# Performance work log

Hardware: AMD Instinct MI355X
Metric: run time of the kernel (lower is better)

## Reference

```python
import jax, jax.numpy as jnp
import numpy as np

ORDER = 5
LOOKAHEAD = 0
NDF = 96  # n_df_bins


def setup_inputs() -> dict:
    key = jax.random.key(0)
    k1, k2, k3 = jax.random.split(key, 3)
    spec = jax.random.normal(k1, (16, 1, 2000, 481, 2), dtype=jnp.float32)
    coefs = jax.random.normal(k2, (16, 2000, ORDER, NDF, 2), dtype=jnp.float32)
    alpha = jax.random.uniform(k3, (16, 2000, 1), dtype=jnp.float32)
    return {"spec": spec, "coefs": coefs, "alpha": alpha}


def reference(spec, coefs, alpha):
    # spec: [B, 1, T, F, 2]; coefs: [B, T, ORDER, NDF, 2]; alpha: [B, T, 1]
    B, _, T, F, _ = spec.shape
    x = spec[:, 0, :, :NDF, :]  # [B, T, NDF, 2]
    # pad time axis: (order - lookahead - 1) before, lookahead after
    xp = jnp.pad(x, ((0, 0), (ORDER - LOOKAHEAD - 1, LOOKAHEAD), (0, 0), (0, 0)))
    # overlapping time windows of length ORDER (loop over small fixed tap count)
    w = jnp.stack([xp[:, k:k + T] for k in range(ORDER)], axis=2)  # [B, T, ORDER, NDF, 2]
    # complex multiply-accumulate per tap, then sum over taps
    re = w[..., 0] * coefs[..., 0] - w[..., 1] * coefs[..., 1]
    im = w[..., 1] * coefs[..., 0] + w[..., 0] * coefs[..., 1]
    spec_f = jnp.stack((re, im), axis=-1).sum(axis=2)  # [B, T, NDF, 2]
    # alpha blend on the low df_bins, copy the rest unchanged
    a = alpha.reshape(B, 1, T, 1, 1)
    mixed = spec_f[:, None] * a + spec[..., :NDF, :] * (1.0 - a)
    return spec.at[..., :NDF, :].set(mixed)
```

## Files before the change

kernel.cpp:

```cpp
#include <hip/hip_runtime.h>

#define BB 16
#define TT 2000
#define FF 481
#define NDF_ 96
#define ORDER_ 5


__global__ __launch_bounds__(256) void df_op_kernel(
    const float* __restrict__ spec,
    const float* __restrict__ coefs,
    const float* __restrict__ alpha,
    float* __restrict__ out)
{
    const int bt = blockIdx.x;
    const int b  = bt / TT;
    const int t  = bt - b * TT;
    const int tid = threadIdx.x;

    const long row = (long)bt * (FF * 2);
    const float a = alpha[bt];
    const float oma = 1.0f - a;

    if (tid < NDF_) {
        const int f = tid;
        float acc_re = 0.0f, acc_im = 0.0f;
        const float2* cbase = (const float2*)(coefs + (long)bt * (ORDER_ * NDF_ * 2) + f * 2);
        #pragma unroll
        for (int k = 0; k < ORDER_; ++k) {
            const int tk = t - (ORDER_ - 1) + k;
            float2 x = make_float2(0.0f, 0.0f);
            if (tk >= 0) {
                x = *(const float2*)(spec + ((long)b * TT + tk) * (FF * 2) + f * 2);
            }
            const float2 c = cbase[k * NDF_];
            acc_re += x.x * c.x - x.y * c.y;
            acc_im += x.y * c.x + x.x * c.y;
        }
        const float2 s = *(const float2*)(spec + row + f * 2);
        float2 o;
        o.x = acc_re * a + s.x * oma;
        o.y = acc_im * a + s.y * oma;
        *(float2*)(out + row + f * 2) = o;
    }

    const float2* src = (const float2*)(spec + row + NDF_ * 2);
    float2*       dst = (float2*)(out + row + NDF_ * 2);
    for (int i = tid; i < (FF - NDF_); i += 256) {
        dst[i] = src[i];
    }
}

extern "C" void kernel_launch(void* const* d_in, const int* in_sizes, int n_in,
                              void* d_out, int out_size, void* d_ws, size_t ws_size,
                              hipStream_t stream) {
    const float* spec  = (const float*)d_in[0];
    const float* coefs = (const float*)d_in[1];
    const float* alpha = (const float*)d_in[2];
    float* out = (float*)d_out;

    dim3 grid(BB * TT);
    dim3 block(256);
    df_op_kernel<<<grid, block, 0, stream>>>(spec, coefs, alpha, out);
}
```

Measured before the change: 285.9 us.

## Process four time rows per block with vectorized float4 loads and copies

Each block now handles four consecutive (b,t) rows instead of one. Each active thread computes two complex bins, loading coefs as float4, and the tail copy of the untouched bins uses float4 moves with parity-aware alignment plus a float2 edge element. This cuts block count, uses all 256 threads, and widens memory transactions so the bandwidth-bound kernel has fewer, larger accesses. The alignment handling for odd rows adds index arithmetic and could misalign if the row stride assumptions change.

```diff
diff --git a/kernel.cpp b/kernel.cpp
--- a/kernel.cpp
+++ b/kernel.cpp
@@ -5,6 +5,10 @@
 #define FF 481
 #define NDF_ 96
 #define ORDER_ 5
+#define RS (FF * 2)
+#define TILE 4
+#define NV (NDF_ / 2)
+#define CSLOTS 193
 
 
 __global__ __launch_bounds__(256) void df_op_kernel(
@@ -13,41 +17,76 @@
     const float* __restrict__ alpha,
     float* __restrict__ out)
 {
-    const int bt = blockIdx.x;
-    const int b  = bt / TT;
-    const int t  = bt - b * TT;
     const int tid = threadIdx.x;
+    const int bt0 = blockIdx.x * TILE;
+    const int b   = bt0 / TT;
+    const int t0  = bt0 - b * TT;
 
-    const long row = (long)bt * (FF * 2);
-    const float a = alpha[bt];
-    const float oma = 1.0f - a;
+    if (tid < TILE * NV) {
+        const int r  = tid / NV;
+        const int v  = tid - r * NV;
+        const int t  = t0 + r;
+        const int bt = bt0 + r;
 
-    if (tid < NDF_) {
-        const int f = tid;
-        float acc_re = 0.0f, acc_im = 0.0f;
-        const float2* cbase = (const float2*)(coefs + (long)bt * (ORDER_ * NDF_ * 2) + f * 2);
+        float2 xs[ORDER_][2];
         #pragma unroll
         for (int k = 0; k < ORDER_; ++k) {
             const int tk = t - (ORDER_ - 1) + k;
-            float2 x = make_float2(0.0f, 0.0f);
             if (tk >= 0) {
-                x = *(const float2*)(spec + ((long)b * TT + tk) * (FF * 2) + f * 2);
+                const float* p = spec + (size_t)(b * TT + tk) * RS + v * 4;
+                xs[k][0] = *(const float2*)p;
+                xs[k][1] = *(const float2*)(p + 2);
+            } else {
+                xs[k][0] = make_float2(0.0f, 0.0f);
+                xs[k][1] = make_float2(0.0f, 0.0f);
             }
-            const float2 c = cbase[k * NDF_];
-            acc_re += x.x * c.x - x.y * c.y;
-            acc_im += x.y * c.x + x.x * c.y;
         }
-        const float2 s = *(const float2*)(spec + row + f * 2);
-        float2 o;
-        o.x = acc_re * a + s.x * oma;
-        o.y = acc_im * a + s.y * oma;
-        *(float2*)(out + row + f * 2) = o;
+
+        const float4* cp = (const float4*)(coefs + (size_t)bt * (ORDER_ * NDF_ * 2)) + v;
+        float4 cs[ORDER_];
+        #pragma unroll
+        for (int k = 0; k < ORDER_; ++k) cs[k] = cp[(size_t)k * NV];
+
+        float2 a0 = make_float2(0.0f, 0.0f);
+        float2 a1 = make_float2(0.0f, 0.0f);
+        #pragma unroll
+        for (int k = 0; k < ORDER_; ++k) {
+            a0.x += xs[k][0].x * cs[k].x - xs[k][0].y * cs[k].y;
+            a0.y += xs[k][0].y * cs[k].x + xs[k][0].x * cs[k].y;
+            a1.x += xs[k][1].x * cs[k].z - xs[k][1].y * cs[k].w;
+            a1.y += xs[k][1].y * cs[k].z + xs[k][1].x * cs[k].w;
+        }
+
+        const float a   = alpha[bt];
+        const float oma = 1.0f - a;
+        float2 o0, o1;
+        o0.x = a0.x * a + xs[ORDER_ - 1][0].x * oma;
+        o0.y = a0.y * a + xs[ORDER_ - 1][0].y * oma;
+        o1.x = a1.x * a + xs[ORDER_ - 1][1].x * oma;
+        o1.y = a1.y * a + xs[ORDER_ - 1][1].y * oma;
+
+        float* op = out + (size_t)bt * RS + v * 4;
+        *(float2*)op       = o0;
+        *(float2*)(op + 2) = o1;
     }
 
-    const float2* src = (const float2*)(spec + row + NDF_ * 2);
-    float2*       dst = (float2*)(out + row + NDF_ * 2);
-    for (int i = tid; i < (FF - NDF_); i += 256) {
-        dst[i] = src[i];
+    #pragma unroll
+    for (int i = 0; i < (TILE * CSLOTS + 255) / 256; ++i) {
+        const int j = tid + i * 256;
+        if (j < TILE * CSLOTS) {
+            const int r  = j / CSLOTS;
+            const int s  = j - r * CSLOTS;
+            const int bt = bt0 + r;
+            const size_t rowf = (size_t)bt * RS;
+            const int odd = bt & 1;
+            if (s < 192) {
+                const size_t off = rowf + (NDF_ * 2) + (odd ? 2 : 0) + (size_t)s * 4;
+                *(float4*)(out + off) = *(const float4*)(spec + off);
+            } else {
+                const size_t off = rowf + (odd ? (NDF_ * 2) : (RS - 2));
+                *(float2*)(out + off) = *(const float2*)(spec + off);
+            }
+        }
     }
 }
 
@@ -59,7 +98,7 @@
     const float* alpha = (const float*)d_in[2];
     float* out = (float*)d_out;
 
-    dim3 grid(BB * TT);
+    dim3 grid((BB * TT) / TILE);
     dim3 block(256);
     df_op_kernel<<<grid, block, 0, stream>>>(spec, coefs, alpha, out);
 }
```

New measurement: 295.0 us. 3.2% more time.
